# Optimization experiments

Hardware: AMD Instinct MI355X
Metric: run time of the kernel (lower is better)

Reference implementation:

```python
import jax, jax.numpy as jnp
import numpy as np


def setup_inputs() -> dict:
    key = jax.random.key(0)
    ks = jax.random.split(key, 6)
    S, B, I, H = 1024, 128, 256, 256
    scale = 1.0 / np.sqrt(H)
    return {
        "x": jax.random.normal(ks[0], (S, B, I), dtype=jnp.float32),
        "h0": jax.random.normal(ks[1], (B, H), dtype=jnp.float32),
        "weight_ih": jax.random.normal(ks[2], (3 * H, I), dtype=jnp.float32) * scale,
        "weight_hh_t": jax.random.normal(ks[3], (H, 3 * H), dtype=jnp.float32) * scale,
        "bias_ih": jax.random.normal(ks[4], (3 * H,), dtype=jnp.float32) * scale,
        "bias_hh": jax.random.normal(ks[5], (3 * H,), dtype=jnp.float32) * scale,
    }


def reference(x, h0, weight_ih, weight_hh_t, bias_ih, bias_hh):
    # x: [S, B, I]; h0: [B, H]
    H = h0.shape[-1]
    # Precompute input-side gate projections for all timesteps: [S, B, 3H]
    x_gates = jnp.einsum("sbi,gi->sbg", x, weight_ih) + bias_ih

    def step(h_prev, xg):  # h_prev: [B, H], xg: [B, 3H]
        gh = h_prev @ weight_hh_t + bias_hh  # [B, 3H]
        r = jax.nn.sigmoid(xg[:, :H] + gh[:, :H])
        z = jax.nn.sigmoid(xg[:, H:2 * H] + gh[:, H:2 * H])
        n = jnp.tanh(xg[:, 2 * H:] + r * gh[:, 2 * H:])
        h_next = (1.0 - z) * n + z * h_prev
        return h_next, h_next

    h_final, h_out = jax.lax.scan(step, h0, x_gates)
    return h_out, h_final
```

## Files before the change

kernel.cpp:

```cpp
#include <hip/hip_runtime.h>
#include <hip/hip_bf16.h>

typedef __attribute__((ext_vector_type(8))) short bf16x8;
typedef __attribute__((ext_vector_type(4))) float f32x4;
typedef __attribute__((ext_vector_type(4))) unsigned short u16x4;

static __device__ __forceinline__ unsigned short f2bf(float f) {
  unsigned u = __builtin_bit_cast(unsigned, f);
  u += 0x7FFFu + ((u >> 16) & 1u);
  return (unsigned short)(u >> 16);
}
static __device__ __forceinline__ float bf2f(unsigned short h) {
  unsigned u = ((unsigned)h) << 16;
  return __builtin_bit_cast(float, u);
}
static __device__ __forceinline__ float sigm(float x) {
  return __builtin_amdgcn_rcpf(1.0f + __builtin_amdgcn_exp2f(x * -1.44269504088896f));
}
static __device__ __forceinline__ float tanh_fast(float x) {
  float e = __builtin_amdgcn_exp2f(x * 2.88539008177793f);
  return 1.0f - 2.0f * __builtin_amdgcn_rcpf(1.0f + e);
}

__global__ __launch_bounds__(256, 2) void gru_xgates(
    const float* __restrict__ x,
    const float* __restrict__ w_ih,
    const float* __restrict__ b_ih,
    const float* __restrict__ b_hh,
    unsigned short* __restrict__ xg)
{
  __shared__ unsigned short Al[128][40];
  __shared__ unsigned short Bl[256][40];

  const int t = threadIdx.x;
  const int lane = t & 63;
  const int w = t >> 6;
  const int l15 = lane & 15;
  const int lhi = lane >> 4;
  const int m0 = blockIdx.y * 128;
  const int g0 = blockIdx.x * 256;
  const int wm = (w >> 1) * 64;
  const int wn = (w & 1) * 128;
  const int rA = t >> 1;
  const int kq = (t & 1) * 16;

  f32x4 acc[4][8];
  #pragma unroll
  for (int mt = 0; mt < 4; ++mt)
    #pragma unroll
    for (int nt = 0; nt < 8; ++nt) acc[mt][nt] = (f32x4){0.f, 0.f, 0.f, 0.f};

  float bias[8];
  #pragma unroll
  for (int nt = 0; nt < 8; ++nt) {
    const int col = g0 + wn + nt * 16 + l15;
    bias[nt] = b_ih[col] + (col < 512 ? b_hh[col] : 0.f);
  }

  for (int kt = 0; kt < 8; ++kt) {
    const int k0 = kt * 32 + kq;
    #pragma unroll
    for (int i = 0; i < 4; ++i) {
      float4 a = *(const float4*)(x + (size_t)(m0 + rA) * 256 + k0 + i * 4);
      *(u16x4*)&Al[rA][kq + i * 4] = (u16x4){f2bf(a.x), f2bf(a.y), f2bf(a.z), f2bf(a.w)};
    }
    #pragma unroll
    for (int h2 = 0; h2 < 2; ++h2) {
      const int rB = rA + h2 * 128;
      #pragma unroll
      for (int i = 0; i < 4; ++i) {
        float4 b = *(const float4*)(w_ih + (size_t)(g0 + rB) * 256 + k0 + i * 4);
        *(u16x4*)&Bl[rB][kq + i * 4] = (u16x4){f2bf(b.x), f2bf(b.y), f2bf(b.z), f2bf(b.w)};
      }
    }
    __syncthreads();

    bf16x8 af[4], bfv[8];
    #pragma unroll
    for (int i = 0; i < 4; ++i) af[i] = *(const bf16x8*)&Al[wm + i * 16 + l15][lhi * 8];
    #pragma unroll
    for (int nt = 0; nt < 8; ++nt) bfv[nt] = *(const bf16x8*)&Bl[wn + nt * 16 + l15][lhi * 8];
    #pragma unroll
    for (int mt = 0; mt < 4; ++mt)
      #pragma unroll
      for (int nt = 0; nt < 8; ++nt)
        acc[mt][nt] = __builtin_amdgcn_mfma_f32_16x16x32_bf16(af[mt], bfv[nt], acc[mt][nt], 0, 0, 0);
    __syncthreads();
  }

  #pragma unroll
  for (int mt = 0; mt < 4; ++mt)
    #pragma unroll
    for (int nt = 0; nt < 8; ++nt)
      #pragma unroll
      for (int q = 0; q < 4; ++q) {
        const int row = m0 + wm + mt * 16 + lhi * 4 + q;
        const int col = g0 + wn + nt * 16 + l15;
        xg[(size_t)row * 768 + col] = f2bf(acc[mt][nt][q] + bias[nt]);
      }
}

__global__ __launch_bounds__(512, 2) void gru_rec(
    const float* __restrict__ hin,
    const float* __restrict__ w_hh,
    const float* __restrict__ b_hh,
    const unsigned short* __restrict__ xg,
    float* __restrict__ hstate,
    float* __restrict__ out,
    int s0, int steps)
{
  __shared__ unsigned short hb[2][4096];
  __shared__ float hpf[16][256];
  __shared__ float bias_lds[256];

  const int t = threadIdx.x;
  const int lane = t & 63;
  const int w = t >> 6;
  const int l15 = lane & 15;
  const int lhi = lane >> 4;
  const int B0 = blockIdx.x * 16;
  const int swz = (l15 & 7) << 4;
  const int cbase = w * 32 + lhi * 4;

  bf16x8 wf[8][6];
  #pragma unroll
  for (int nt = 0; nt < 6; ++nt) {
    const int col = (nt >> 1) * 256 + w * 32 + (nt & 1) * 16 + l15;
    #pragma unroll
    for (int kt = 0; kt < 8; ++kt) {
      bf16x8 v;
      #pragma unroll
      for (int e = 0; e < 8; ++e)
        v[e] = (short)f2bf(w_hh[(size_t)(kt * 32 + lhi * 8 + e) * 768 + col]);
      wf[kt][nt] = v;
    }
  }

  if (t < 256) bias_lds[t] = b_hh[512 + t];

  #pragma unroll
  for (int half = 0; half < 2; ++half) {
    const int c = cbase + half * 16;
    f32x4 h = *(const f32x4*)(hin + (size_t)(B0 + l15) * 256 + c);
    *(f32x4*)((char*)hpf + l15 * 1024 + ((c * 4) ^ swz)) = h;
    *(u16x4*)((char*)hb[0] + l15 * 512 + ((c * 2) ^ swz)) =
        (u16x4){f2bf(h[0]), f2bf(h[1]), f2bf(h[2]), f2bf(h[3])};
  }

  const unsigned short* xp = xg + (size_t)(B0 + l15) * 768 + cbase;
  u16x4 xgv[6];
  #pragma unroll
  for (int g = 0; g < 3; ++g)
    #pragma unroll
    for (int half = 0; half < 2; ++half)
      xgv[g * 2 + half] = *(const u16x4*)(xp + g * 256 + half * 16);

  float* op = out + (size_t)s0 * 32768 + (size_t)(B0 + l15) * 256 + cbase;
  __syncthreads();

  #pragma unroll 1
  for (int s = 0; s < steps; ++s) {
    const char* hcur = (const char*)hb[s & 1];
    char* hnxt = (char*)hb[(s & 1) ^ 1];

    f32x4 acc[6];
    acc[0] = acc[1] = acc[2] = acc[3] = (f32x4){0.f, 0.f, 0.f, 0.f};
    acc[4] = *(const f32x4*)&bias_lds[cbase];
    acc[5] = *(const f32x4*)&bias_lds[cbase + 16];

    #pragma unroll
    for (int kt = 0; kt < 8; ++kt) {
      bf16x8 hf = *(const bf16x8*)(hcur + l15 * 512 + ((kt * 64 + lhi * 16) ^ swz));
      #pragma unroll
      for (int nt = 0; nt < 6; ++nt)
        acc[nt] = __builtin_amdgcn_mfma_f32_16x16x32_bf16(wf[kt][nt], hf, acc[nt], 0, 0, 0);
    }

    const unsigned short* xpn = xp + (s + 1 < steps ? 98304 : 0);

    #pragma unroll
    for (int half = 0; half < 2; ++half) {
      const int c = cbase + half * 16;
      f32x4 hp = *(const f32x4*)((const char*)hpf + l15 * 1024 + ((c * 4) ^ swz));
      f32x4 hn;
      #pragma unroll
      for (int q = 0; q < 4; ++q) {
        const float r = sigm(bf2f(xgv[half][q]) + acc[half][q]);
        const float z = sigm(bf2f(xgv[2 + half][q]) + acc[2 + half][q]);
        const float n = tanh_fast(bf2f(xgv[4 + half][q]) + r * acc[4 + half][q]);
        hn[q] = n + z * (hp[q] - n);
      }
      xgv[half]     = *(const u16x4*)(xpn + half * 16);
      xgv[2 + half] = *(const u16x4*)(xpn + 256 + half * 16);
      xgv[4 + half] = *(const u16x4*)(xpn + 512 + half * 16);

      *(f32x4*)((char*)hpf + l15 * 1024 + ((c * 4) ^ swz)) = hn;
      *(u16x4*)(hnxt + l15 * 512 + ((c * 2) ^ swz)) =
          (u16x4){f2bf(hn[0]), f2bf(hn[1]), f2bf(hn[2]), f2bf(hn[3])};
      *(f32x4*)(op + half * 16) = hn;
    }

    xp = xpn;
    op += 32768;
    __syncthreads();
  }

  #pragma unroll
  for (int half = 0; half < 2; ++half) {
    const int c = cbase + half * 16;
    f32x4 h = *(const f32x4*)((const char*)hpf + l15 * 1024 + ((c * 4) ^ swz));
    *(f32x4*)(hstate + (size_t)(B0 + l15) * 256 + c) = h;
    *(f32x4*)(out + (size_t)1024 * 32768 + (size_t)(B0 + l15) * 256 + c) = h;
  }
}

extern "C" void kernel_launch(void* const* d_in, const int* in_sizes, int n_in,
                              void* d_out, int out_size, void* d_ws, size_t ws_size,
                              hipStream_t stream) {
  const float* x    = (const float*)d_in[0];
  const float* h0   = (const float*)d_in[1];
  const float* w_ih = (const float*)d_in[2];
  const float* w_hh = (const float*)d_in[3];
  const float* b_ih = (const float*)d_in[4];
  const float* b_hh = (const float*)d_in[5];
  float* out = (float*)d_out;

  float* hstate = (float*)d_ws;
  unsigned short* xg = (unsigned short*)((char*)d_ws + 131072);
  const size_t avail = ws_size > 131072 ? ws_size - 131072 : 0;

  int C = 1024;
  while (C > 1 && (size_t)C * 196608ull > avail) C >>= 1;

  for (int c0 = 0; c0 < 1024; c0 += C) {
    gru_xgates<<<dim3(3, C), 256, 0, stream>>>(x + (size_t)c0 * 32768, w_ih, b_ih, b_hh, xg);
    gru_rec<<<dim3(8), 512, 0, stream>>>(c0 == 0 ? h0 : hstate, w_hh, b_hh, xg,
                                         hstate, out, c0, C);
  }
}
```

Baseline: 3.650 ms.

## Keep fp32 hidden state in registers and re-layout bf16 h buffer in LDS

Drops the fp32 hidden-state LDS array and keeps each thread's previous h in registers, since every thread owns the same columns across steps. The bf16 h buffer is re-laid out as 32-bit words with a rotated slot mapping, so each thread writes two dwords and reads four scattered dwords per k-tile. The r/z input-gate values now preload the MFMA accumulators, and next-step xg loads are issued before the matmul to hide global latency. This trades one wide LDS read per k-tile for four narrow reads, aiming to cut LDS traffic and bank conflicts on the serial recurrence path.

```diff
diff --git a/kernel.cpp b/kernel.cpp
--- a/kernel.cpp
+++ b/kernel.cpp
@@ -109,8 +109,7 @@
     float* __restrict__ out,
     int s0, int steps)
 {
-  __shared__ unsigned short hb[2][4096];
-  __shared__ float hpf[16][256];
+  __shared__ unsigned hb[2][2048];
   __shared__ float bias_lds[256];
 
   const int t = threadIdx.x;
@@ -119,7 +118,6 @@
   const int l15 = lane & 15;
   const int lhi = lane >> 4;
   const int B0 = blockIdx.x * 16;
-  const int swz = (l15 & 7) << 4;
   const int cbase = w * 32 + lhi * 4;
 
   bf16x8 wf[8][6];
@@ -138,67 +136,103 @@
 
   if (t < 256) bias_lds[t] = b_hh[512 + t];
 
+  int rb[4];
+  #pragma unroll
+  for (int j = 0; j < 4; ++j) {
+    const int row = lhi * 2 + (j >> 1);
+    const int slot = (l15 + 16 * (j & 1) + 4 * (j >> 1) + 8 * lhi) & 31;
+    rb[j] = (row * 32 + slot) * 4;
+  }
+  int wb[2][2];
   #pragma unroll
   for (int half = 0; half < 2; ++half) {
-    const int c = cbase + half * 16;
-    f32x4 h = *(const f32x4*)(hin + (size_t)(B0 + l15) * 256 + c);
-    *(f32x4*)((char*)hpf + l15 * 1024 + ((c * 4) ^ swz)) = h;
-    *(u16x4*)((char*)hb[0] + l15 * 512 + ((c * 2) ^ swz)) =
-        (u16x4){f2bf(h[0]), f2bf(h[1]), f2bf(h[2]), f2bf(h[3])};
+    const int row = w * 8 + lhi + half * 4;
+    const int sl0 = (l15 + 4 * (lhi & 1) + 8 * (((lhi >> 1) + half * 2) & 3)) & 31;
+    wb[half][0] = (row * 32 + sl0) * 4;
+    wb[half][1] = (row * 32 + ((sl0 + 16) & 31)) * 4;
+  }
+
+  f32x4 hp[2];
+  {
+    char* hw = (char*)hb[0];
+    #pragma unroll
+    for (int half = 0; half < 2; ++half) {
+      hp[half] = *(const f32x4*)(hin + (size_t)(B0 + l15) * 256 + cbase + half * 16);
+      unsigned d0 = (unsigned)f2bf(hp[half][0]) | ((unsigned)f2bf(hp[half][1]) << 16);
+      unsigned d1 = (unsigned)f2bf(hp[half][2]) | ((unsigned)f2bf(hp[half][3]) << 16);
+      *(unsigned*)(hw + wb[half][0]) = d0;
+      *(unsigned*)(hw + wb[half][1]) = d1;
+    }
   }
 
   const unsigned short* xp = xg + (size_t)(B0 + l15) * 768 + cbase;
-  u16x4 xgv[6];
-  #pragma unroll
-  for (int g = 0; g < 3; ++g)
-    #pragma unroll
-    for (int half = 0; half < 2; ++half)
-      xgv[g * 2 + half] = *(const u16x4*)(xp + g * 256 + half * 16);
+  u16x4 xrz[4];
+  u16x4 xn_c[2], xn_n[2];
+  #pragma unroll
+  for (int half = 0; half < 2; ++half) {
+    xrz[half]     = *(const u16x4*)(xp + half * 16);
+    xrz[2 + half] = *(const u16x4*)(xp + 256 + half * 16);
+    xn_c[half]    = *(const u16x4*)(xp + 512 + half * 16);
+  }
 
   float* op = out + (size_t)s0 * 32768 + (size_t)(B0 + l15) * 256 + cbase;
   __syncthreads();
 
   #pragma unroll 1
   for (int s = 0; s < steps; ++s) {
-    const char* hcur = (const char*)hb[s & 1];
-    char* hnxt = (char*)hb[(s & 1) ^ 1];
+    const char* hr = (const char*)hb[s & 1];
+    char* hw = (char*)hb[(s & 1) ^ 1];
 
     f32x4 acc[6];
-    acc[0] = acc[1] = acc[2] = acc[3] = (f32x4){0.f, 0.f, 0.f, 0.f};
-    acc[4] = *(const f32x4*)&bias_lds[cbase];
-    acc[5] = *(const f32x4*)&bias_lds[cbase + 16];
+    #pragma unroll
+    for (int half = 0; half < 2; ++half) {
+      acc[half]     = (f32x4){bf2f(xrz[half][0]), bf2f(xrz[half][1]),
+                              bf2f(xrz[half][2]), bf2f(xrz[half][3])};
+      acc[2 + half] = (f32x4){bf2f(xrz[2 + half][0]), bf2f(xrz[2 + half][1]),
+                              bf2f(xrz[2 + half][2]), bf2f(xrz[2 + half][3])};
+      acc[4 + half] = *(const f32x4*)&bias_lds[cbase + half * 16];
+    }
+
+    const unsigned short* xpn = xp + (s + 1 < steps ? 98304 : 0);
+    #pragma unroll
+    for (int half = 0; half < 2; ++half) {
+      xrz[half]     = *(const u16x4*)(xpn + half * 16);
+      xrz[2 + half] = *(const u16x4*)(xpn + 256 + half * 16);
+      xn_n[half]    = *(const u16x4*)(xpn + 512 + half * 16);
+    }
 
     #pragma unroll
     for (int kt = 0; kt < 8; ++kt) {
-      bf16x8 hf = *(const bf16x8*)(hcur + l15 * 512 + ((kt * 64 + lhi * 16) ^ swz));
+      int4 hd;
+      hd.x = *(const int*)(hr + rb[0] + kt * 1024);
+      hd.y = *(const int*)(hr + rb[1] + kt * 1024);
+      hd.z = *(const int*)(hr + rb[2] + kt * 1024);
+      hd.w = *(const int*)(hr + rb[3] + kt * 1024);
+      const bf16x8 hf = __builtin_bit_cast(bf16x8, hd);
       #pragma unroll
       for (int nt = 0; nt < 6; ++nt)
         acc[nt] = __builtin_amdgcn_mfma_f32_16x16x32_bf16(wf[kt][nt], hf, acc[nt], 0, 0, 0);
     }
 
-    const unsigned short* xpn = xp + (s + 1 < steps ? 98304 : 0);
-
-    #pragma unroll
-    for (int half = 0; half < 2; ++half) {
-      const int c = cbase + half * 16;
-      f32x4 hp = *(const f32x4*)((const char*)hpf + l15 * 1024 + ((c * 4) ^ swz));
+    #pragma unroll
+    for (int half = 0; half < 2; ++half) {
       f32x4 hn;
       #pragma unroll
       for (int q = 0; q < 4; ++q) {
-        const float r = sigm(bf2f(xgv[half][q]) + acc[half][q]);
-        const float z = sigm(bf2f(xgv[2 + half][q]) + acc[2 + half][q]);
-        const float n = tanh_fast(bf2f(xgv[4 + half][q]) + r * acc[4 + half][q]);
-        hn[q] = n + z * (hp[q] - n);
+        const float r = sigm(acc[half][q]);
+        const float z = sigm(acc[2 + half][q]);
+        const float n = tanh_fast(bf2f(xn_c[half][q]) + r * acc[4 + half][q]);
+        hn[q] = n + z * (hp[half][q] - n);
       }
-      xgv[half]     = *(const u16x4*)(xpn + half * 16);
-      xgv[2 + half] = *(const u16x4*)(xpn + 256 + half * 16);
-      xgv[4 + half] = *(const u16x4*)(xpn + 512 + half * 16);
-
-      *(f32x4*)((char*)hpf + l15 * 1024 + ((c * 4) ^ swz)) = hn;
-      *(u16x4*)(hnxt + l15 * 512 + ((c * 2) ^ swz)) =
-          (u16x4){f2bf(hn[0]), f2bf(hn[1]), f2bf(hn[2]), f2bf(hn[3])};
+      hp[half] = hn;
+      unsigned d0 = (unsigned)f2bf(hn[0]) | ((unsigned)f2bf(hn[1]) << 16);
+      unsigned d1 = (unsigned)f2bf(hn[2]) | ((unsigned)f2bf(hn[3]) << 16);
+      *(unsigned*)(hw + wb[half][0]) = d0;
+      *(unsigned*)(hw + wb[half][1]) = d1;
       *(f32x4*)(op + half * 16) = hn;
     }
+    xn_c[0] = xn_n[0];
+    xn_c[1] = xn_n[1];
 
     xp = xpn;
     op += 32768;
@@ -208,9 +242,8 @@
   #pragma unroll
   for (int half = 0; half < 2; ++half) {
     const int c = cbase + half * 16;
-    f32x4 h = *(const f32x4*)((const char*)hpf + l15 * 1024 + ((c * 4) ^ swz));
-    *(f32x4*)(hstate + (size_t)(B0 + l15) * 256 + c) = h;
-    *(f32x4*)(out + (size_t)1024 * 32768 + (size_t)(B0 + l15) * 256 + c) = h;
+    *(f32x4*)(hstate + (size_t)(B0 + l15) * 256 + c) = hp[half];
+    *(f32x4*)(out + (size_t)1024 * 32768 + (size_t)(B0 + l15) * 256 + c) = hp[half];
   }
 }
 
```

After: 3.636 ms. No clear change (-0.4%).
